# Kernel tuning notes

Measured on AMD Instinct MI355X. Metric: run time of the kernel, lower is better.

The kernel has to match this reference:

```python
import jax, jax.numpy as jnp
import numpy as np

N_NODES = 50000
N_EDGES = 800000  # undirected edge count E0
D_FEAT = 64
K_STEPS = 10
LAMBDA = 3.0


def setup_inputs() -> dict:
    key = jax.random.key(0)
    k1, k2, k3 = jax.random.split(key, 3)
    x = jax.random.normal(k1, (N_NODES, D_FEAT), dtype=jnp.float32)
    edge_src = jax.random.randint(k2, (N_EDGES,), 0, N_NODES)
    edge_dst = jax.random.randint(k3, (N_EDGES,), 0, N_NODES)
    return {"x": x, "edge_src": edge_src, "edge_dst": edge_dst}


def _forward(x, edge_src, edge_dst):
    N, D = x.shape
    # --- symmetric adjacency (directed edge list, both orientations) ---
    row = jnp.concatenate([edge_src, edge_dst])
    col = jnp.concatenate([edge_dst, edge_src])
    # degree with self loops (fill_diag/add_self_loops weight 1), shared by
    # gcn_norm and inc_norm in the original code
    deg = jax.ops.segment_sum(jnp.ones(row.shape[0], x.dtype), row, num_segments=N) + 1.0
    dis = deg ** -0.5  # deg_inv_sqrt, [N]
    # gcn-normalized adjacency weights D^-1/2 (A+I) D^-1/2
    w = dis[row] * dis[col]          # off-diagonal edge weights [2*E0]
    w_self = dis * dis               # self-loop weights [N]

    def adj_mv(v):  # edge_index @ v
        return jax.ops.segment_sum(w[:, None] * v[col], row, num_segments=N) + w_self[:, None] * v

    # --- normalized incidence matrix (one row per undirected edge) ---
    r = jnp.maximum(edge_src, edge_dst)  # row_index after row>=col mask
    c = jnp.minimum(edge_src, edge_dst)
    a = dis[r]  # +1 entry scaled by deg_inv_sqrt of column r
    b = dis[c]  # -1 entry scaled by deg_inv_sqrt of column c

    def inc_mv(v):  # inc_mat @ v -> [E0, D]
        return a[:, None] * v[r] - b[:, None] * v[c]

    def incT_mv(z):  # inc_mat.t() @ z -> [N, D]
        return (jax.ops.segment_sum(a[:, None] * z, r, num_segments=N)
                - jax.ops.segment_sum(b[:, None] * z, c, num_segments=N))

    def l21_projection(z):
        rn = jnp.linalg.norm(z, axis=1)                 # row L2 norms [E0]
        s = jnp.minimum(rn, LAMBDA)
        s = jnp.where(rn > 0, s / jnp.where(rn > 0, rn, 1.0), s)
        return s[:, None] * z

    hh = x
    z0 = jnp.zeros((edge_src.shape[0], D), x.dtype)

    def step(carry, _):
        xk, zk = carry
        y = 0.25 * hh + 0.75 * adj_mv(xk)
        x_bar = y - 0.25 * incT_mv(zk)
        z_bar = zk + 2.0 * inc_mv(x_bar)
        zk = l21_projection(z_bar)
        xk = y - 0.25 * incT_mv(zk)
        return (xk, zk), None

    (xK, _), _ = jax.lax.scan(step, (x, z0), None, length=K_STEPS)
    return xK


def reference(x, edge_src, edge_dst):
    return _forward(x, edge_src, edge_dst)
```

## Files before the change

### kernel.cpp

```cpp
#include <hip/hip_runtime.h>
#include <hip/hip_fp16.h>
#include <math.h>

constexpr int NN = 50000;
constexpr int NE = 800000;
constexpr int KS = 10;
constexpr float LAM = 3.0f;

constexpr int SCAN_NB = (NN + 255) / 256;

struct __align__(16) EInfo { int r; float a; int c; float b; };


__global__ __launch_bounds__(256) void countRC_kernel(
    const int* __restrict__ src, const int* __restrict__ dst,
    int* __restrict__ cR, int* __restrict__ cC) {
  int e = blockIdx.x * 256 + threadIdx.x;
  if (e >= NE) return;
  int s = src[e], d = dst[e];
  int r = s > d ? s : d;
  int c = s > d ? d : s;
  atomicAdd(&cR[r], 1);
  atomicAdd(&cC[c], 1);
}

__global__ __launch_bounds__(256) void dis_kernel(
    const int* __restrict__ cR, const int* __restrict__ cC,
    float* __restrict__ dis) {
  int i = blockIdx.x * 256 + threadIdx.x;
  if (i < NN) dis[i] = 1.0f / sqrtf((float)(cR[i] + cC[i] + 1));
}

__global__ __launch_bounds__(256) void half_copy_kernel(
    const float* __restrict__ X, __half* __restrict__ XH) {
  int i = blockIdx.x * 256 + threadIdx.x;
  if (i >= NN * 16) return;
  float4 v = ((const float4*)X)[i];
  __half2 h0 = __floats2half2_rn(v.x, v.y);
  __half2 h1 = __floats2half2_rn(v.z, v.w);
  uint2 o;
  o.x = *(const unsigned*)&h0;
  o.y = *(const unsigned*)&h1;
  ((uint2*)XH)[i] = o;
}


__global__ __launch_bounds__(256) void scanA_kernel(
    const int* __restrict__ cnt, int* __restrict__ bsum) {
  __shared__ int sm[256];
  int t = threadIdx.x;
  int i = blockIdx.x * 256 + t;
  int v = (i < NN) ? cnt[i] : 0;
  sm[t] = v;
  __syncthreads();
  for (int off = 128; off > 0; off >>= 1) {
    if (t < off) sm[t] += sm[t + off];
    __syncthreads();
  }
  if (t == 0) bsum[blockIdx.x] = sm[0];
}

__global__ __launch_bounds__(256) void scanB_kernel(
    int* __restrict__ bsum, int* __restrict__ boff) {
  __shared__ int sm[256];
  int t = threadIdx.x;
  int v = (t < SCAN_NB) ? bsum[t] : 0;
  sm[t] = v;
  __syncthreads();
  for (int off = 1; off < 256; off <<= 1) {
    int a = (t >= off) ? sm[t - off] : 0;
    __syncthreads();
    sm[t] += a;
    __syncthreads();
  }
  if (t < SCAN_NB) boff[t] = sm[t] - v;
}

__global__ __launch_bounds__(256) void scanC_kernel(
    const int* __restrict__ cnt, const int* __restrict__ boff,
    int* __restrict__ ptr, int* __restrict__ cur) {
  __shared__ int sm[256];
  int t = threadIdx.x;
  int i = blockIdx.x * 256 + t;
  int v = (i < NN) ? cnt[i] : 0;
  sm[t] = v;
  __syncthreads();
  for (int off = 1; off < 256; off <<= 1) {
    int a = (t >= off) ? sm[t - off] : 0;
    __syncthreads();
    sm[t] += a;
    __syncthreads();
  }
  if (i < NN) {
    int ex = boff[blockIdx.x] + sm[t] - v;
    ptr[i] = ex;
    cur[i] = ex;
    if (i == NN - 1) ptr[NN] = ex + v;
  }
}

__global__ __launch_bounds__(256) void sortscatter_kernel(
    const int* __restrict__ src, const int* __restrict__ dst,
    const float* __restrict__ dis,
    int* __restrict__ urR, int* __restrict__ uC,
    EInfo* __restrict__ rcab, int2* __restrict__ cEnt) {
  int e = blockIdx.x * 256 + threadIdx.x;
  if (e >= NE) return;
  int s = src[e], d = dst[e];
  int r = s > d ? s : d;
  int c = s > d ? d : s;
  int p = atomicAdd(&urR[r], 1);
  EInfo ei; ei.r = r; ei.a = dis[r]; ei.c = c; ei.b = dis[c];
  rcab[p] = ei;
  int q = atomicAdd(&uC[c], 1);
  cEnt[q] = make_int2(r, p);
}


template <int FIRST>
__global__ __launch_bounds__(256) void adj_kernel(
    const float* __restrict__ Xk, const __half* __restrict__ XH,
    const float* __restrict__ H, const float* __restrict__ U,
    const float* __restrict__ dis,
    const int* __restrict__ rPtr, const int* __restrict__ cPtr,
    const int2* __restrict__ cEnt, const EInfo* __restrict__ rcab,
    float* __restrict__ XB, __half* __restrict__ XBh) {
  int w = (int)((blockIdx.x * 256u + threadIdx.x) >> 6);
  if (w >= NN) return;
  int lane = threadIdx.x & 63;
  int g = lane >> 4, l = lane & 15;
  const uint2* XH2 = (const uint2*)XH;
  const uint2* rc2 = (const uint2*)rcab;
  int rb = rPtr[w], lenR = rPtr[w + 1] - rb;
  int cb = cPtr[w], lenC = cPtr[w + 1] - cb;
  int total = lenR + lenC;
  int lr1 = lenR > 0 ? lenR - 1 : 0;
  int lc1 = lenC > 0 ? lenC - 1 : 0;
  float ax = 0.f, ay = 0.f, az = 0.f, aw = 0.f;

#define ADJ_FETCH(T, NB, WT)                                         \
  {                                                                  \
    int tr = (T) < lr1 ? (T) : lr1;                                  \
    int tc = (T) - lenR; tc = tc > 0 ? tc : 0; tc = tc < lc1 ? tc : lc1; \
    uint2 rc = rc2[2 * (rb + tr) + 1];                               \
    int2 ce = cEnt[cb + tc];                                         \
    bool isR = (T) < lenR;                                           \
    NB = isR ? (int)rc.x : ce.x;                                     \
    WT = isR ? __uint_as_float(rc.y) : dis[ce.x];                    \
  }
#define ADJ_ACC(XV, W)                                               \
  {                                                                  \
    float2 p = __half22float2(*(const __half2*)&XV.x);               \
    float2 q = __half22float2(*(const __half2*)&XV.y);               \
    ax = fmaf(W, p.x, ax); ay = fmaf(W, p.y, ay);                    \
    az = fmaf(W, q.x, az); aw = fmaf(W, q.y, aw);                    \
  }

  int t = g;
  for (; t + 12 < total; t += 16) {
    int n0, n1, n2, n3; float w0, w1, w2, w3;
    ADJ_FETCH(t, n0, w0);
    ADJ_FETCH(t + 4, n1, w1);
    ADJ_FETCH(t + 8, n2, w2);
    ADJ_FETCH(t + 12, n3, w3);
    uint2 x0 = XH2[n0 * 16 + l];
    uint2 x1 = XH2[n1 * 16 + l];
    uint2 x2 = XH2[n2 * 16 + l];
    uint2 x3 = XH2[n3 * 16 + l];
    ADJ_ACC(x0, w0);
    ADJ_ACC(x1, w1);
    ADJ_ACC(x2, w2);
    ADJ_ACC(x3, w3);
  }
  for (; t < total; t += 4) {
    int n0; float w0;
    ADJ_FETCH(t, n0, w0);
    uint2 x0 = XH2[n0 * 16 + l];
    ADJ_ACC(x0, w0);
  }
#undef ADJ_FETCH
#undef ADJ_ACC

  ax += __shfl_xor(ax, 16, 64); ay += __shfl_xor(ay, 16, 64);
  az += __shfl_xor(az, 16, 64); aw += __shfl_xor(aw, 16, 64);
  ax += __shfl_xor(ax, 32, 64); ay += __shfl_xor(ay, 32, 64);
  az += __shfl_xor(az, 32, 64); aw += __shfl_xor(aw, 32, 64);
  if (g == 0) {
    float di = dis[w];
    int idx = w * 16 + l;
    float4 xs = ((const float4*)Xk)[idx];
    float4 h4 = ((const float4*)H)[idx];
    float4 y4;
    y4.x = 0.25f * h4.x + 0.75f * di * fmaf(di, xs.x, ax);
    y4.y = 0.25f * h4.y + 0.75f * di * fmaf(di, xs.y, ay);
    y4.z = 0.25f * h4.z + 0.75f * di * fmaf(di, xs.z, az);
    y4.w = 0.25f * h4.w + 0.75f * di * fmaf(di, xs.w, aw);
    float4 xb;
    if (FIRST) {
      xb = y4;
    } else {
      float4 u4 = ((const float4*)U)[idx];
      xb.x = y4.x - 0.25f * u4.x;
      xb.y = y4.y - 0.25f * u4.y;
      xb.z = y4.z - 0.25f * u4.z;
      xb.w = y4.w - 0.25f * u4.w;
    }
    ((float4*)XB)[idx] = xb;
    __half2 hb0 = __floats2half2_rn(xb.x, xb.y);
    __half2 hb1 = __floats2half2_rn(xb.z, xb.w);
    uint2 ob;
    ob.x = *(const unsigned*)&hb0;
    ob.y = *(const unsigned*)&hb1;
    ((uint2*)XBh)[idx] = ob;
  }
}

template <int FIRST>
__global__ __launch_bounds__(256) void zstep_kernel(
    __half* __restrict__ Z, const __half* __restrict__ XBh,
    const EInfo* __restrict__ rcab) {
  int w = (int)((blockIdx.x * 256u + threadIdx.x) >> 6);
  int base = w * 8;
  if (base >= NE) return;
  int lane = threadIdx.x & 63;
  int g = lane >> 4, l = lane & 15;
  int e0 = base + g, e1 = base + g + 4;
  EInfo ei0 = rcab[e0];
  EInfo ei1 = rcab[e1];
  const uint2* X2 = (const uint2*)XBh;
  uint2* Z2 = (uint2*)Z;
  int zi0 = e0 * 16 + l, zi1 = e1 * 16 + l;
  uint2 xr0u = X2[ei0.r * 16 + l];
  uint2 xc0u = X2[ei0.c * 16 + l];
  uint2 xr1u = X2[ei1.r * 16 + l];
  uint2 xc1u = X2[ei1.c * 16 + l];
  float2 xr0a = __half22float2(*(const __half2*)&xr0u.x);
  float2 xr0b = __half22float2(*(const __half2*)&xr0u.y);
  float2 xc0a = __half22float2(*(const __half2*)&xc0u.x);
  float2 xc0b = __half22float2(*(const __half2*)&xc0u.y);
  float2 xr1a = __half22float2(*(const __half2*)&xr1u.x);
  float2 xr1b = __half22float2(*(const __half2*)&xr1u.y);
  float2 xc1a = __half22float2(*(const __half2*)&xc1u.x);
  float2 xc1b = __half22float2(*(const __half2*)&xc1u.y);
  float zx0, zy0, zz0, zw0, zx1, zy1, zz1, zw1;
  if (FIRST) {
    zx0 = zy0 = zz0 = zw0 = 0.f;
    zx1 = zy1 = zz1 = zw1 = 0.f;
  } else {
    uint2 zu0 = Z2[zi0];
    uint2 zu1 = Z2[zi1];
    float2 f0 = __half22float2(*(const __half2*)&zu0.x);
    float2 f1 = __half22float2(*(const __half2*)&zu0.y);
    zx0 = f0.x; zy0 = f0.y; zz0 = f1.x; zw0 = f1.y;
    f0 = __half22float2(*(const __half2*)&zu1.x);
    f1 = __half22float2(*(const __half2*)&zu1.y);
    zx1 = f0.x; zy1 = f0.y; zz1 = f1.x; zw1 = f1.y;
  }
  zx0 += 2.0f * (ei0.a * xr0a.x - ei0.b * xc0a.x);
  zy0 += 2.0f * (ei0.a * xr0a.y - ei0.b * xc0a.y);
  zz0 += 2.0f * (ei0.a * xr0b.x - ei0.b * xc0b.x);
  zw0 += 2.0f * (ei0.a * xr0b.y - ei0.b * xc0b.y);
  zx1 += 2.0f * (ei1.a * xr1a.x - ei1.b * xc1a.x);
  zy1 += 2.0f * (ei1.a * xr1a.y - ei1.b * xc1a.y);
  zz1 += 2.0f * (ei1.a * xr1b.x - ei1.b * xc1b.x);
  zw1 += 2.0f * (ei1.a * xr1b.y - ei1.b * xc1b.y);
  float s0 = zx0 * zx0 + zy0 * zy0 + zz0 * zz0 + zw0 * zw0;
  float s1 = zx1 * zx1 + zy1 * zy1 + zz1 * zz1 + zw1 * zw1;
  s0 += __shfl_xor(s0, 1, 64); s1 += __shfl_xor(s1, 1, 64);
  s0 += __shfl_xor(s0, 2, 64); s1 += __shfl_xor(s1, 2, 64);
  s0 += __shfl_xor(s0, 4, 64); s1 += __shfl_xor(s1, 4, 64);
  s0 += __shfl_xor(s0, 8, 64); s1 += __shfl_xor(s1, 8, 64);
  float rn0 = sqrtf(s0), rn1 = sqrtf(s1);
  float sc0 = (rn0 > LAM) ? (LAM / rn0) : 1.0f;
  float sc1 = (rn1 > LAM) ? (LAM / rn1) : 1.0f;
  __half2 a0 = __floats2half2_rn(sc0 * zx0, sc0 * zy0);
  __half2 b0 = __floats2half2_rn(sc0 * zz0, sc0 * zw0);
  __half2 a1 = __floats2half2_rn(sc1 * zx1, sc1 * zy1);
  __half2 b1 = __floats2half2_rn(sc1 * zz1, sc1 * zw1);
  uint2 o0, o1;
  o0.x = *(const unsigned*)&a0; o0.y = *(const unsigned*)&b0;
  o1.x = *(const unsigned*)&a1; o1.y = *(const unsigned*)&b1;
  Z2[zi0] = o0;
  Z2[zi1] = o1;
}

template <int FIRST, int LAST>
__global__ __launch_bounds__(256) void incT_kernel(
    const __half* __restrict__ Z, const float* __restrict__ XB,
    const float* __restrict__ dis,
    const int* __restrict__ rPtr, const int* __restrict__ cPtr,
    const int2* __restrict__ cEnt,
    float* __restrict__ U, float* __restrict__ Xout,
    __half* __restrict__ XH) {
  int w = (int)((blockIdx.x * 256u + threadIdx.x) >> 6);
  if (w >= NN) return;
  int lane = threadIdx.x & 63;
  int g = lane >> 4, l = lane & 15;
  const uint2* Z2 = (const uint2*)Z;
  int rb = rPtr[w], lenR = rPtr[w + 1] - rb;
  int cb = cPtr[w], lenC = cPtr[w + 1] - cb;
  int total = lenR + lenC;
  int lc1 = lenC > 0 ? lenC - 1 : 0;
  float ax = 0.f, ay = 0.f, az = 0.f, aw = 0.f;

#define INCT_FETCH(T, E, SG)                                         \
  {                                                                  \
    int tc = (T) - lenR; tc = tc > 0 ? tc : 0; tc = tc < lc1 ? tc : lc1; \
    int2 ce = cEnt[cb + tc];                                         \
    bool isR = (T) < lenR;                                           \
    E = isR ? (rb + (T)) : ce.y;                                     \
    SG = isR ? 1.0f : -1.0f;                                         \
  }

  int t = g;
  for (; t + 12 < total; t += 16) {
    int e0, e1, e2, e3; float s0, s1, s2, s3;
    INCT_FETCH(t, e0, s0);
    INCT_FETCH(t + 4, e1, s1);
    INCT_FETCH(t + 8, e2, s2);
    INCT_FETCH(t + 12, e3, s3);
    uint2 zu0 = Z2[e0 * 16 + l];
    uint2 zu1 = Z2[e1 * 16 + l];
    uint2 zu2 = Z2[e2 * 16 + l];
    uint2 zu3 = Z2[e3 * 16 + l];
    float2 a0 = __half22float2(*(const __half2*)&zu0.x);
    float2 b0 = __half22float2(*(const __half2*)&zu0.y);
    float2 a1 = __half22float2(*(const __half2*)&zu1.x);
    float2 b1 = __half22float2(*(const __half2*)&zu1.y);
    float2 a2 = __half22float2(*(const __half2*)&zu2.x);
    float2 b2 = __half22float2(*(const __half2*)&zu2.y);
    float2 a3 = __half22float2(*(const __half2*)&zu3.x);
    float2 b3 = __half22float2(*(const __half2*)&zu3.y);
    ax = fmaf(s0, a0.x, ax); ay = fmaf(s0, a0.y, ay);
    az = fmaf(s0, b0.x, az); aw = fmaf(s0, b0.y, aw);
    ax = fmaf(s1, a1.x, ax); ay = fmaf(s1, a1.y, ay);
    az = fmaf(s1, b1.x, az); aw = fmaf(s1, b1.y, aw);
    ax = fmaf(s2, a2.x, ax); ay = fmaf(s2, a2.y, ay);
    az = fmaf(s2, b2.x, az); aw = fmaf(s2, b2.y, aw);
    ax = fmaf(s3, a3.x, ax); ay = fmaf(s3, a3.y, ay);
    az = fmaf(s3, b3.x, az); aw = fmaf(s3, b3.y, aw);
  }
  for (; t < total; t += 4) {
    int e0; float s0;
    INCT_FETCH(t, e0, s0);
    uint2 zu0 = Z2[e0 * 16 + l];
    float2 a0 = __half22float2(*(const __half2*)&zu0.x);
    float2 b0 = __half22float2(*(const __half2*)&zu0.y);
    ax = fmaf(s0, a0.x, ax); ay = fmaf(s0, a0.y, ay);
    az = fmaf(s0, b0.x, az); aw = fmaf(s0, b0.y, aw);
  }
#undef INCT_FETCH

  ax += __shfl_xor(ax, 16, 64); ay += __shfl_xor(ay, 16, 64);
  az += __shfl_xor(az, 16, 64); aw += __shfl_xor(aw, 16, 64);
  ax += __shfl_xor(ax, 32, 64); ay += __shfl_xor(ay, 32, 64);
  az += __shfl_xor(az, 32, 64); aw += __shfl_xor(aw, 32, 64);
  if (g == 0) {
    float di = dis[w];
    int idx = w * 16 + l;
    float4 u;
    u.x = di * ax; u.y = di * ay; u.z = di * az; u.w = di * aw;
    float4 xb = ((const float4*)XB)[idx];
    float4 y4;
    if (FIRST) {
      y4 = xb;
    } else {
      float4 uo = ((const float4*)U)[idx];
      y4.x = xb.x + 0.25f * uo.x;
      y4.y = xb.y + 0.25f * uo.y;
      y4.z = xb.z + 0.25f * uo.z;
      y4.w = xb.w + 0.25f * uo.w;
    }
    if (!LAST) ((float4*)U)[idx] = u;
    float4 o;
    o.x = y4.x - 0.25f * u.x;
    o.y = y4.y - 0.25f * u.y;
    o.z = y4.z - 0.25f * u.z;
    o.w = y4.w - 0.25f * u.w;
    ((float4*)Xout)[idx] = o;
    if (!LAST) {
      __half2 h0 = __floats2half2_rn(o.x, o.y);
      __half2 h1 = __floats2half2_rn(o.z, o.w);
      uint2 oh;
      oh.x = *(const unsigned*)&h0;
      oh.y = *(const unsigned*)&h1;
      ((uint2*)XH)[idx] = oh;
    }
  }
}


extern "C" void kernel_launch(void* const* d_in, const int* in_sizes, int n_in,
                              void* d_out, int out_size, void* d_ws, size_t ws_size,
                              hipStream_t stream) {
  const float* x  = (const float*)d_in[0];
  const int* esrc = (const int*)d_in[1];
  const int* edst = (const int*)d_in[2];
  float* out = (float*)d_out;

  char* base = (char*)d_ws;
  size_t off = 0;
  auto carve = [&](size_t bytes) -> void* {
    void* p = base + off;
    off += (bytes + 255) & ~(size_t)255;
    return p;
  };
  __half* Z   = (__half*)carve((size_t)NE * 64 * 2);
  float* XK   = (float*)carve((size_t)NN * 64 * 4);
  float* XB   = (float*)carve((size_t)NN * 64 * 4);
  float* U    = (float*)carve((size_t)NN * 64 * 4);
  __half* XH  = (__half*)carve((size_t)NN * 64 * 2);
  __half* XBh = (__half*)carve((size_t)NN * 64 * 2);
  float* dis = (float*)carve((size_t)NN * 4);
  int* cR  = (int*)carve((size_t)NN * 4);
  int* cC  = (int*)carve((size_t)NN * 4);
  int* rPtr = (int*)carve((size_t)(NN + 1) * 4);
  int* cPtr = (int*)carve((size_t)(NN + 1) * 4);
  int* urR = (int*)carve((size_t)NN * 4);
  int* uC  = (int*)carve((size_t)NN * 4);
  int* bsum = (int*)carve((size_t)SCAN_NB * 4);
  int* boff = (int*)carve((size_t)SCAN_NB * 4);
  EInfo* rcab = (EInfo*)carve((size_t)NE * 16);
  int2* cEnt = (int2*)carve((size_t)NE * 8);
  (void)ws_size; (void)in_sizes; (void)n_in; (void)out_size;

  hipMemsetAsync(cR, 0, NN * 4, stream);
  hipMemsetAsync(cC, 0, NN * 4, stream);

  const int edgeGrid = (NE + 255) / 256;
  countRC_kernel<<<edgeGrid, 256, 0, stream>>>(esrc, edst, cR, cC);
  dis_kernel<<<(NN + 255) / 256, 256, 0, stream>>>(cR, cC, dis);
  half_copy_kernel<<<(NN * 16 + 255) / 256, 256, 0, stream>>>(x, XH);
  scanA_kernel<<<SCAN_NB, 256, 0, stream>>>(cR, bsum);
  scanB_kernel<<<1, 256, 0, stream>>>(bsum, boff);
  scanC_kernel<<<SCAN_NB, 256, 0, stream>>>(cR, boff, rPtr, urR);
  scanA_kernel<<<SCAN_NB, 256, 0, stream>>>(cC, bsum);
  scanB_kernel<<<1, 256, 0, stream>>>(bsum, boff);
  scanC_kernel<<<SCAN_NB, 256, 0, stream>>>(cC, boff, cPtr, uC);
  sortscatter_kernel<<<edgeGrid, 256, 0, stream>>>(esrc, edst, dis, urR, uC,
                                                   rcab, cEnt);

  const int nodeBlocks = NN * 64 / 256;
  const int edgeBlocks = (NE / 8) * 64 / 256;

  for (int k = 0; k < KS; ++k) {
    const float* xk = (k == 0) ? x : XK;
    if (k == 0)
      adj_kernel<1><<<nodeBlocks, 256, 0, stream>>>(xk, XH, x, U, dis, rPtr,
                                                    cPtr, cEnt, rcab, XB, XBh);
    else
      adj_kernel<0><<<nodeBlocks, 256, 0, stream>>>(xk, XH, x, U, dis, rPtr,
                                                    cPtr, cEnt, rcab, XB, XBh);

    if (k == 0)
      zstep_kernel<1><<<edgeBlocks, 256, 0, stream>>>(Z, XBh, rcab);
    else
      zstep_kernel<0><<<edgeBlocks, 256, 0, stream>>>(Z, XBh, rcab);

    float* xout = (k == KS - 1) ? out : XK;
    if (k == 0)
      incT_kernel<1, 0><<<nodeBlocks, 256, 0, stream>>>(Z, XB, dis, rPtr, cPtr,
                                                        cEnt, U, xout, XH);
    else if (k == KS - 1)
      incT_kernel<0, 1><<<nodeBlocks, 256, 0, stream>>>(Z, XB, dis, rPtr, cPtr,
                                                        cEnt, U, xout, XH);
    else
      incT_kernel<0, 0><<<nodeBlocks, 256, 0, stream>>>(Z, XB, dis, rPtr, cPtr,
                                                        cEnt, U, xout, XH);
  }
}
```

Baseline: 1.427 ms.

## Fuse z-update with row-side incidence sum and split adj gather into feature halves

```diff
diff --git a/kernel.cpp b/kernel.cpp
--- a/kernel.cpp
+++ b/kernel.cpp
@@ -8,8 +8,7 @@
 constexpr float LAM = 3.0f;
 
 constexpr int SCAN_NB = (NN + 255) / 256;
-
-struct __align__(16) EInfo { int r; float a; int c; float b; };
+constexpr int NODE_NB = NN * 64 / 256;
 
 
 __global__ __launch_bounds__(256) void countRC_kernel(
@@ -32,7 +31,8 @@
 }
 
 __global__ __launch_bounds__(256) void half_copy_kernel(
-    const float* __restrict__ X, __half* __restrict__ XH) {
+    const float* __restrict__ X, __half* __restrict__ XHlo,
+    __half* __restrict__ XHhi) {
   int i = blockIdx.x * 256 + threadIdx.x;
   if (i >= NN * 16) return;
   float4 v = ((const float4*)X)[i];
@@ -41,7 +41,9 @@
   uint2 o;
   o.x = *(const unsigned*)&h0;
   o.y = *(const unsigned*)&h1;
-  ((uint2*)XH)[i] = o;
+  int w = i >> 4, f4 = i & 15;
+  __half* dst = (f4 < 8) ? XHlo : XHhi;
+  ((uint2*)dst)[w * 8 + (f4 & 7)] = o;
 }
 
 
@@ -103,15 +105,14 @@
     const int* __restrict__ src, const int* __restrict__ dst,
     const float* __restrict__ dis,
     int* __restrict__ urR, int* __restrict__ uC,
-    EInfo* __restrict__ rcab, int2* __restrict__ cEnt) {
+    int2* __restrict__ cb8, int2* __restrict__ cEnt) {
   int e = blockIdx.x * 256 + threadIdx.x;
   if (e >= NE) return;
   int s = src[e], d = dst[e];
   int r = s > d ? s : d;
   int c = s > d ? d : s;
   int p = atomicAdd(&urR[r], 1);
-  EInfo ei; ei.r = r; ei.a = dis[r]; ei.c = c; ei.b = dis[c];
-  rcab[p] = ei;
+  cb8[p] = make_int2(c, __float_as_int(dis[c]));
   int q = atomicAdd(&uC[c], 1);
   cEnt[q] = make_int2(r, p);
 }
@@ -119,18 +120,19 @@
 
 template <int FIRST>
 __global__ __launch_bounds__(256) void adj_kernel(
-    const float* __restrict__ Xk, const __half* __restrict__ XH,
+    const __half* __restrict__ XHlo, const __half* __restrict__ XHhi,
     const float* __restrict__ H, const float* __restrict__ U,
     const float* __restrict__ dis,
     const int* __restrict__ rPtr, const int* __restrict__ cPtr,
-    const int2* __restrict__ cEnt, const EInfo* __restrict__ rcab,
+    const int2* __restrict__ cEnt, const int2* __restrict__ cb8,
     float* __restrict__ XB, __half* __restrict__ XBh) {
-  int w = (int)((blockIdx.x * 256u + threadIdx.x) >> 6);
+  int bid = blockIdx.x;
+  int half = (bid >= NODE_NB) ? 1 : 0;
+  int w = (int)(((unsigned)(bid - half * NODE_NB) * 256u + threadIdx.x) >> 6);
   if (w >= NN) return;
   int lane = threadIdx.x & 63;
-  int g = lane >> 4, l = lane & 15;
-  const uint2* XH2 = (const uint2*)XH;
-  const uint2* rc2 = (const uint2*)rcab;
+  int g = lane >> 3, l = lane & 7;
+  const uint2* XH2 = (const uint2*)(half ? XHhi : XHlo);
   int rb = rPtr[w], lenR = rPtr[w + 1] - rb;
   int cb = cPtr[w], lenC = cPtr[w + 1] - cb;
   int total = lenR + lenC;
@@ -142,11 +144,11 @@
   {                                                                  \
     int tr = (T) < lr1 ? (T) : lr1;                                  \
     int tc = (T) - lenR; tc = tc > 0 ? tc : 0; tc = tc < lc1 ? tc : lc1; \
-    uint2 rc = rc2[2 * (rb + tr) + 1];                               \
+    int2 rcv = cb8[rb + tr];                                         \
     int2 ce = cEnt[cb + tc];                                         \
     bool isR = (T) < lenR;                                           \
-    NB = isR ? (int)rc.x : ce.x;                                     \
-    WT = isR ? __uint_as_float(rc.y) : dis[ce.x];                    \
+    NB = isR ? rcv.x : ce.x;                                         \
+    WT = isR ? __int_as_float(rcv.y) : dis[ce.x];                    \
   }
 #define ADJ_ACC(XV, W)                                               \
   {                                                                  \
@@ -157,44 +159,42 @@
   }
 
   int t = g;
-  for (; t + 12 < total; t += 16) {
-    int n0, n1, n2, n3; float w0, w1, w2, w3;
+  for (; t + 8 < total; t += 16) {
+    int n0, n1; float w0, w1;
     ADJ_FETCH(t, n0, w0);
-    ADJ_FETCH(t + 4, n1, w1);
-    ADJ_FETCH(t + 8, n2, w2);
-    ADJ_FETCH(t + 12, n3, w3);
-    uint2 x0 = XH2[n0 * 16 + l];
-    uint2 x1 = XH2[n1 * 16 + l];
-    uint2 x2 = XH2[n2 * 16 + l];
-    uint2 x3 = XH2[n3 * 16 + l];
+    ADJ_FETCH(t + 8, n1, w1);
+    uint2 x0 = XH2[n0 * 8 + l];
+    uint2 x1 = XH2[n1 * 8 + l];
     ADJ_ACC(x0, w0);
     ADJ_ACC(x1, w1);
-    ADJ_ACC(x2, w2);
-    ADJ_ACC(x3, w3);
-  }
-  for (; t < total; t += 4) {
+  }
+  for (; t < total; t += 8) {
     int n0; float w0;
     ADJ_FETCH(t, n0, w0);
-    uint2 x0 = XH2[n0 * 16 + l];
+    uint2 x0 = XH2[n0 * 8 + l];
     ADJ_ACC(x0, w0);
   }
 #undef ADJ_FETCH
 #undef ADJ_ACC
 
+  ax += __shfl_xor(ax, 8, 64); ay += __shfl_xor(ay, 8, 64);
+  az += __shfl_xor(az, 8, 64); aw += __shfl_xor(aw, 8, 64);
   ax += __shfl_xor(ax, 16, 64); ay += __shfl_xor(ay, 16, 64);
   az += __shfl_xor(az, 16, 64); aw += __shfl_xor(aw, 16, 64);
   ax += __shfl_xor(ax, 32, 64); ay += __shfl_xor(ay, 32, 64);
   az += __shfl_xor(az, 32, 64); aw += __shfl_xor(aw, 32, 64);
   if (g == 0) {
     float di = dis[w];
-    int idx = w * 16 + l;
-    float4 xs = ((const float4*)Xk)[idx];
+    int idx = w * 16 + half * 8 + l;
+    uint2 xsu = XH2[w * 8 + l];
+    float2 xsa = __half22float2(*(const __half2*)&xsu.x);
+    float2 xsb = __half22float2(*(const __half2*)&xsu.y);
     float4 h4 = ((const float4*)H)[idx];
     float4 y4;
-    y4.x = 0.25f * h4.x + 0.75f * di * fmaf(di, xs.x, ax);
-    y4.y = 0.25f * h4.y + 0.75f * di * fmaf(di, xs.y, ay);
-    y4.z = 0.25f * h4.z + 0.75f * di * fmaf(di, xs.z, az);
-    y4.w = 0.25f * h4.w + 0.75f * di * fmaf(di, xs.w, aw);
+    y4.x = 0.25f * h4.x + 0.75f * di * fmaf(di, xsa.x, ax);
+    y4.y = 0.25f * h4.y + 0.75f * di * fmaf(di, xsa.y, ay);
+    y4.z = 0.25f * h4.z + 0.75f * di * fmaf(di, xsb.x, az);
+    y4.w = 0.25f * h4.w + 0.75f * di * fmaf(di, xsb.y, aw);
     float4 xb;
     if (FIRST) {
       xb = y4;
@@ -216,109 +216,89 @@
 }
 
 template <int FIRST>
-__global__ __launch_bounds__(256) void zstep_kernel(
+__global__ __launch_bounds__(256) void zupd_kernel(
     __half* __restrict__ Z, const __half* __restrict__ XBh,
-    const EInfo* __restrict__ rcab) {
+    const float* __restrict__ dis,
+    const int* __restrict__ rPtr, const int2* __restrict__ cb8,
+    float* __restrict__ U1) {
   int w = (int)((blockIdx.x * 256u + threadIdx.x) >> 6);
-  int base = w * 8;
-  if (base >= NE) return;
+  if (w >= NN) return;
   int lane = threadIdx.x & 63;
   int g = lane >> 4, l = lane & 15;
-  int e0 = base + g, e1 = base + g + 4;
-  EInfo ei0 = rcab[e0];
-  EInfo ei1 = rcab[e1];
   const uint2* X2 = (const uint2*)XBh;
   uint2* Z2 = (uint2*)Z;
-  int zi0 = e0 * 16 + l, zi1 = e1 * 16 + l;
-  uint2 xr0u = X2[ei0.r * 16 + l];
-  uint2 xc0u = X2[ei0.c * 16 + l];
-  uint2 xr1u = X2[ei1.r * 16 + l];
-  uint2 xc1u = X2[ei1.c * 16 + l];
-  float2 xr0a = __half22float2(*(const __half2*)&xr0u.x);
-  float2 xr0b = __half22float2(*(const __half2*)&xr0u.y);
-  float2 xc0a = __half22float2(*(const __half2*)&xc0u.x);
-  float2 xc0b = __half22float2(*(const __half2*)&xc0u.y);
-  float2 xr1a = __half22float2(*(const __half2*)&xr1u.x);
-  float2 xr1b = __half22float2(*(const __half2*)&xr1u.y);
-  float2 xc1a = __half22float2(*(const __half2*)&xc1u.x);
-  float2 xc1b = __half22float2(*(const __half2*)&xc1u.y);
-  float zx0, zy0, zz0, zw0, zx1, zy1, zz1, zw1;
-  if (FIRST) {
-    zx0 = zy0 = zz0 = zw0 = 0.f;
-    zx1 = zy1 = zz1 = zw1 = 0.f;
-  } else {
-    uint2 zu0 = Z2[zi0];
-    uint2 zu1 = Z2[zi1];
-    float2 f0 = __half22float2(*(const __half2*)&zu0.x);
-    float2 f1 = __half22float2(*(const __half2*)&zu0.y);
-    zx0 = f0.x; zy0 = f0.y; zz0 = f1.x; zw0 = f1.y;
-    f0 = __half22float2(*(const __half2*)&zu1.x);
-    f1 = __half22float2(*(const __half2*)&zu1.y);
-    zx1 = f0.x; zy1 = f0.y; zz1 = f1.x; zw1 = f1.y;
-  }
-  zx0 += 2.0f * (ei0.a * xr0a.x - ei0.b * xc0a.x);
-  zy0 += 2.0f * (ei0.a * xr0a.y - ei0.b * xc0a.y);
-  zz0 += 2.0f * (ei0.a * xr0b.x - ei0.b * xc0b.x);
-  zw0 += 2.0f * (ei0.a * xr0b.y - ei0.b * xc0b.y);
-  zx1 += 2.0f * (ei1.a * xr1a.x - ei1.b * xc1a.x);
-  zy1 += 2.0f * (ei1.a * xr1a.y - ei1.b * xc1a.y);
-  zz1 += 2.0f * (ei1.a * xr1b.x - ei1.b * xc1b.x);
-  zw1 += 2.0f * (ei1.a * xr1b.y - ei1.b * xc1b.y);
-  float s0 = zx0 * zx0 + zy0 * zy0 + zz0 * zz0 + zw0 * zw0;
-  float s1 = zx1 * zx1 + zy1 * zy1 + zz1 * zz1 + zw1 * zw1;
-  s0 += __shfl_xor(s0, 1, 64); s1 += __shfl_xor(s1, 1, 64);
-  s0 += __shfl_xor(s0, 2, 64); s1 += __shfl_xor(s1, 2, 64);
-  s0 += __shfl_xor(s0, 4, 64); s1 += __shfl_xor(s1, 4, 64);
-  s0 += __shfl_xor(s0, 8, 64); s1 += __shfl_xor(s1, 8, 64);
-  float rn0 = sqrtf(s0), rn1 = sqrtf(s1);
-  float sc0 = (rn0 > LAM) ? (LAM / rn0) : 1.0f;
-  float sc1 = (rn1 > LAM) ? (LAM / rn1) : 1.0f;
-  __half2 a0 = __floats2half2_rn(sc0 * zx0, sc0 * zy0);
-  __half2 b0 = __floats2half2_rn(sc0 * zz0, sc0 * zw0);
-  __half2 a1 = __floats2half2_rn(sc1 * zx1, sc1 * zy1);
-  __half2 b1 = __floats2half2_rn(sc1 * zz1, sc1 * zw1);
-  uint2 o0, o1;
-  o0.x = *(const unsigned*)&a0; o0.y = *(const unsigned*)&b0;
-  o1.x = *(const unsigned*)&a1; o1.y = *(const unsigned*)&b1;
-  Z2[zi0] = o0;
-  Z2[zi1] = o1;
+  int rb = rPtr[w], re = rPtr[w + 1];
+  float a = dis[w];
+  uint2 xwu = X2[w * 16 + l];
+  float2 xwa = __half22float2(*(const __half2*)&xwu.x);
+  float2 xwb = __half22float2(*(const __half2*)&xwu.y);
+  float sx = 0.f, sy = 0.f, sz = 0.f, sw = 0.f;
+  for (int e = rb + g; e < re; e += 4) {
+    int2 cbv = cb8[e];
+    int c = cbv.x;
+    float b = __int_as_float(cbv.y);
+    uint2 xcu = X2[c * 16 + l];
+    float2 xca = __half22float2(*(const __half2*)&xcu.x);
+    float2 xcb = __half22float2(*(const __half2*)&xcu.y);
+    float zx, zy, zz, zw;
+    if (FIRST) {
+      zx = zy = zz = zw = 0.f;
+    } else {
+      uint2 zu = Z2[e * 16 + l];
+      float2 f0 = __half22float2(*(const __half2*)&zu.x);
+      float2 f1 = __half22float2(*(const __half2*)&zu.y);
+      zx = f0.x; zy = f0.y; zz = f1.x; zw = f1.y;
+    }
+    zx += 2.0f * (a * xwa.x - b * xca.x);
+    zy += 2.0f * (a * xwa.y - b * xca.y);
+    zz += 2.0f * (a * xwb.x - b * xcb.x);
+    zw += 2.0f * (a * xwb.y - b * xcb.y);
+    float ss = zx * zx + zy * zy + zz * zz + zw * zw;
+    ss += __shfl_xor(ss, 1, 64);
+    ss += __shfl_xor(ss, 2, 64);
+    ss += __shfl_xor(ss, 4, 64);
+    ss += __shfl_xor(ss, 8, 64);
+    float rn = sqrtf(ss);
+    float sc = (rn > LAM) ? (LAM / rn) : 1.0f;
+    zx *= sc; zy *= sc; zz *= sc; zw *= sc;
+    __half2 o0 = __floats2half2_rn(zx, zy);
+    __half2 o1 = __floats2half2_rn(zz, zw);
+    uint2 outu;
+    outu.x = *(const unsigned*)&o0;
+    outu.y = *(const unsigned*)&o1;
+    Z2[e * 16 + l] = outu;
+    sx += zx; sy += zy; sz += zz; sw += zw;
+  }
+  sx += __shfl_xor(sx, 16, 64); sy += __shfl_xor(sy, 16, 64);
+  sz += __shfl_xor(sz, 16, 64); sw += __shfl_xor(sw, 16, 64);
+  sx += __shfl_xor(sx, 32, 64); sy += __shfl_xor(sy, 32, 64);
+  sz += __shfl_xor(sz, 32, 64); sw += __shfl_xor(sw, 32, 64);
+  if (g == 0) {
+    ((float4*)U1)[w * 16 + l] = make_float4(sx, sy, sz, sw);
+  }
 }
 
 template <int FIRST, int LAST>
-__global__ __launch_bounds__(256) void incT_kernel(
+__global__ __launch_bounds__(256) void cside_kernel(
     const __half* __restrict__ Z, const float* __restrict__ XB,
     const float* __restrict__ dis,
-    const int* __restrict__ rPtr, const int* __restrict__ cPtr,
-    const int2* __restrict__ cEnt,
-    float* __restrict__ U, float* __restrict__ Xout,
-    __half* __restrict__ XH) {
+    const int* __restrict__ cPtr, const int2* __restrict__ cEnt,
+    const float* __restrict__ U1, float* __restrict__ U,
+    float* __restrict__ Xout, __half* __restrict__ XHlo,
+    __half* __restrict__ XHhi) {
   int w = (int)((blockIdx.x * 256u + threadIdx.x) >> 6);
   if (w >= NN) return;
   int lane = threadIdx.x & 63;
   int g = lane >> 4, l = lane & 15;
   const uint2* Z2 = (const uint2*)Z;
-  int rb = rPtr[w], lenR = rPtr[w + 1] - rb;
-  int cb = cPtr[w], lenC = cPtr[w + 1] - cb;
-  int total = lenR + lenC;
-  int lc1 = lenC > 0 ? lenC - 1 : 0;
-  float ax = 0.f, ay = 0.f, az = 0.f, aw = 0.f;
-
-#define INCT_FETCH(T, E, SG)                                         \
-  {                                                                  \
-    int tc = (T) - lenR; tc = tc > 0 ? tc : 0; tc = tc < lc1 ? tc : lc1; \
-    int2 ce = cEnt[cb + tc];                                         \
-    bool isR = (T) < lenR;                                           \
-    E = isR ? (rb + (T)) : ce.y;                                     \
-    SG = isR ? 1.0f : -1.0f;                                         \
-  }
-
-  int t = g;
-  for (; t + 12 < total; t += 16) {
-    int e0, e1, e2, e3; float s0, s1, s2, s3;
-    INCT_FETCH(t, e0, s0);
-    INCT_FETCH(t + 4, e1, s1);
-    INCT_FETCH(t + 8, e2, s2);
-    INCT_FETCH(t + 12, e3, s3);
+  int cb = cPtr[w], ce = cPtr[w + 1];
+  float sx = 0.f, sy = 0.f, sz = 0.f, sw = 0.f;
+  int j = cb + g;
+  for (; j + 12 < ce; j += 16) {
+    int e0 = cEnt[j].y;
+    int e1 = cEnt[j + 4].y;
+    int e2 = cEnt[j + 8].y;
+    int e3 = cEnt[j + 12].y;
     uint2 zu0 = Z2[e0 * 16 + l];
     uint2 zu1 = Z2[e1 * 16 + l];
     uint2 zu2 = Z2[e2 * 16 + l];
@@ -331,35 +311,31 @@
     float2 b2 = __half22float2(*(const __half2*)&zu2.y);
     float2 a3 = __half22float2(*(const __half2*)&zu3.x);
     float2 b3 = __half22float2(*(const __half2*)&zu3.y);
-    ax = fmaf(s0, a0.x, ax); ay = fmaf(s0, a0.y, ay);
-    az = fmaf(s0, b0.x, az); aw = fmaf(s0, b0.y, aw);
-    ax = fmaf(s1, a1.x, ax); ay = fmaf(s1, a1.y, ay);
-    az = fmaf(s1, b1.x, az); aw = fmaf(s1, b1.y, aw);
-    ax = fmaf(s2, a2.x, ax); ay = fmaf(s2, a2.y, ay);
-    az = fmaf(s2, b2.x, az); aw = fmaf(s2, b2.y, aw);
-    ax = fmaf(s3, a3.x, ax); ay = fmaf(s3, a3.y, ay);
-    az = fmaf(s3, b3.x, az); aw = fmaf(s3, b3.y, aw);
-  }
-  for (; t < total; t += 4) {
-    int e0; float s0;
-    INCT_FETCH(t, e0, s0);
+    sx += a0.x + a1.x + a2.x + a3.x;
+    sy += a0.y + a1.y + a2.y + a3.y;
+    sz += b0.x + b1.x + b2.x + b3.x;
+    sw += b0.y + b1.y + b2.y + b3.y;
+  }
+  for (; j < ce; j += 4) {
+    int e0 = cEnt[j].y;
     uint2 zu0 = Z2[e0 * 16 + l];
     float2 a0 = __half22float2(*(const __half2*)&zu0.x);
     float2 b0 = __half22float2(*(const __half2*)&zu0.y);
-    ax = fmaf(s0, a0.x, ax); ay = fmaf(s0, a0.y, ay);
-    az = fmaf(s0, b0.x, az); aw = fmaf(s0, b0.y, aw);
-  }
-#undef INCT_FETCH
-
-  ax += __shfl_xor(ax, 16, 64); ay += __shfl_xor(ay, 16, 64);
-  az += __shfl_xor(az, 16, 64); aw += __shfl_xor(aw, 16, 64);
-  ax += __shfl_xor(ax, 32, 64); ay += __shfl_xor(ay, 32, 64);
-  az += __shfl_xor(az, 32, 64); aw += __shfl_xor(aw, 32, 64);
+    sx += a0.x; sy += a0.y; sz += b0.x; sw += b0.y;
+  }
+  sx += __shfl_xor(sx, 16, 64); sy += __shfl_xor(sy, 16, 64);
+  sz += __shfl_xor(sz, 16, 64); sw += __shfl_xor(sw, 16, 64);
+  sx += __shfl_xor(sx, 32, 64); sy += __shfl_xor(sy, 32, 64);
+  sz += __shfl_xor(sz, 32, 64); sw += __shfl_xor(sw, 32, 64);
   if (g == 0) {
     float di = dis[w];
     int idx = w * 16 + l;
+    float4 u1 = ((const float4*)U1)[idx];
     float4 u;
-    u.x = di * ax; u.y = di * ay; u.z = di * az; u.w = di * aw;
+    u.x = di * (u1.x - sx);
+    u.y = di * (u1.y - sy);
+    u.z = di * (u1.z - sz);
+    u.w = di * (u1.w - sw);
     float4 xb = ((const float4*)XB)[idx];
     float4 y4;
     if (FIRST) {
@@ -371,20 +347,22 @@
       y4.z = xb.z + 0.25f * uo.z;
       y4.w = xb.w + 0.25f * uo.w;
     }
-    if (!LAST) ((float4*)U)[idx] = u;
     float4 o;
     o.x = y4.x - 0.25f * u.x;
     o.y = y4.y - 0.25f * u.y;
     o.z = y4.z - 0.25f * u.z;
     o.w = y4.w - 0.25f * u.w;
-    ((float4*)Xout)[idx] = o;
-    if (!LAST) {
+    if (LAST) {
+      ((float4*)Xout)[idx] = o;
+    } else {
+      ((float4*)U)[idx] = u;
       __half2 h0 = __floats2half2_rn(o.x, o.y);
       __half2 h1 = __floats2half2_rn(o.z, o.w);
       uint2 oh;
       oh.x = *(const unsigned*)&h0;
       oh.y = *(const unsigned*)&h1;
-      ((uint2*)XH)[idx] = oh;
+      __half* dst = (l < 8) ? XHlo : XHhi;
+      ((uint2*)dst)[w * 8 + (l & 7)] = oh;
     }
   }
 }
@@ -405,12 +383,13 @@
     off += (bytes + 255) & ~(size_t)255;
     return p;
   };
-  __half* Z   = (__half*)carve((size_t)NE * 64 * 2);
-  float* XK   = (float*)carve((size_t)NN * 64 * 4);
-  float* XB   = (float*)carve((size_t)NN * 64 * 4);
-  float* U    = (float*)carve((size_t)NN * 64 * 4);
-  __half* XH  = (__half*)carve((size_t)NN * 64 * 2);
-  __half* XBh = (__half*)carve((size_t)NN * 64 * 2);
+  __half* Z    = (__half*)carve((size_t)NE * 64 * 2);
+  float* XB    = (float*)carve((size_t)NN * 64 * 4);
+  float* U     = (float*)carve((size_t)NN * 64 * 4);
+  float* U1    = (float*)carve((size_t)NN * 64 * 4);
+  __half* XHlo = (__half*)carve((size_t)NN * 32 * 2);
+  __half* XHhi = (__half*)carve((size_t)NN * 32 * 2);
+  __half* XBh  = (__half*)carve((size_t)NN * 64 * 2);
   float* dis = (float*)carve((size_t)NN * 4);
   int* cR  = (int*)carve((size_t)NN * 4);
   int* cC  = (int*)carve((size_t)NN * 4);
@@ -420,7 +399,7 @@
   int* uC  = (int*)carve((size_t)NN * 4);
   int* bsum = (int*)carve((size_t)SCAN_NB * 4);
   int* boff = (int*)carve((size_t)SCAN_NB * 4);
-  EInfo* rcab = (EInfo*)carve((size_t)NE * 16);
+  int2* cb8  = (int2*)carve((size_t)NE * 8);
   int2* cEnt = (int2*)carve((size_t)NE * 8);
   (void)ws_size; (void)in_sizes; (void)n_in; (void)out_size;
 
@@ -430,7 +409,7 @@
   const int edgeGrid = (NE + 255) / 256;
   countRC_kernel<<<edgeGrid, 256, 0, stream>>>(esrc, edst, cR, cC);
   dis_kernel<<<(NN + 255) / 256, 256, 0, stream>>>(cR, cC, dis);
-  half_copy_kernel<<<(NN * 16 + 255) / 256, 256, 0, stream>>>(x, XH);
+  half_copy_kernel<<<(NN * 16 + 255) / 256, 256, 0, stream>>>(x, XHlo, XHhi);
   scanA_kernel<<<SCAN_NB, 256, 0, stream>>>(cR, bsum);
   scanB_kernel<<<1, 256, 0, stream>>>(bsum, boff);
   scanC_kernel<<<SCAN_NB, 256, 0, stream>>>(cR, boff, rPtr, urR);
@@ -438,34 +417,31 @@
   scanB_kernel<<<1, 256, 0, stream>>>(bsum, boff);
   scanC_kernel<<<SCAN_NB, 256, 0, stream>>>(cC, boff, cPtr, uC);
   sortscatter_kernel<<<edgeGrid, 256, 0, stream>>>(esrc, edst, dis, urR, uC,
-                                                   rcab, cEnt);
-
-  const int nodeBlocks = NN * 64 / 256;
-  const int edgeBlocks = (NE / 8) * 64 / 256;
+                                                   cb8, cEnt);
 
   for (int k = 0; k < KS; ++k) {
-    const float* xk = (k == 0) ? x : XK;
     if (k == 0)
-      adj_kernel<1><<<nodeBlocks, 256, 0, stream>>>(xk, XH, x, U, dis, rPtr,
-                                                    cPtr, cEnt, rcab, XB, XBh);
+      adj_kernel<1><<<2 * NODE_NB, 256, 0, stream>>>(XHlo, XHhi, x, U, dis,
+                                                     rPtr, cPtr, cEnt, cb8,
+                                                     XB, XBh);
     else
-      adj_kernel<0><<<nodeBlocks, 256, 0, stream>>>(xk, XH, x, U, dis, rPtr,
-                                                    cPtr, cEnt, rcab, XB, XBh);
+      adj_kernel<0><<<2 * NODE_NB, 256, 0, stream>>>(XHlo, XHhi, x, U, dis,
+                                                     rPtr, cPtr, cEnt, cb8,
+                                                     XB, XBh);
 
     if (k == 0)
-      zstep_kernel<1><<<edgeBlocks, 256, 0, stream>>>(Z, XBh, rcab);
+      zupd_kernel<1><<<NODE_NB, 256, 0, stream>>>(Z, XBh, dis, rPtr, cb8, U1);
     else
-      zstep_kernel<0><<<edgeBlocks, 256, 0, stream>>>(Z, XBh, rcab);
-
-    float* xout = (k == KS - 1) ? out : XK;
+      zupd_kernel<0><<<NODE_NB, 256, 0, stream>>>(Z, XBh, dis, rPtr, cb8, U1);
+
     if (k == 0)
-      incT_kernel<1, 0><<<nodeBlocks, 256, 0, stream>>>(Z, XB, dis, rPtr, cPtr,
-                                                        cEnt, U, xout, XH);
+      cside_kernel<1, 0><<<NODE_NB, 256, 0, stream>>>(Z, XB, dis, cPtr, cEnt,
+                                                      U1, U, out, XHlo, XHhi);
     else if (k == KS - 1)
-      incT_kernel<0, 1><<<nodeBlocks, 256, 0, stream>>>(Z, XB, dis, rPtr, cPtr,
-                                                        cEnt, U, xout, XH);
+      cside_kernel<0, 1><<<NODE_NB, 256, 0, stream>>>(Z, XB, dis, cPtr, cEnt,
+                                                      U1, U, out, XHlo, XHhi);
     else
-      incT_kernel<0, 0><<<nodeBlocks, 256, 0, stream>>>(Z, XB, dis, rPtr, cPtr,
-                                                        cEnt, U, xout, XH);
-  }
-}
+      cside_kernel<0, 0><<<NODE_NB, 256, 0, stream>>>(Z, XB, dis, cPtr, cEnt,
+                                                      U1, U, out, XHlo, XHhi);
+  }
+}
```

Measured after the change: 1.548 ms. 1.09x slower.
